# Kernel tuning notes

Hardware: AMD Instinct MI355X
Metric: run time of the kernel (lower is better)

The kernel has to match this reference:

```python
import jax, jax.numpy as jnp
import numpy as np

EMBED = 1024
SEQ = 2048
HEAD = 64
BATCH = 4


def setup_inputs() -> dict:
    key = jax.random.key(0)
    k1, k2, k3, k4 = jax.random.split(key, 4)
    # small weight scale to keep pre-softmax logits (scaled by sqrt(c)=32) stable
    x = jax.random.normal(k1, (BATCH, SEQ, EMBED), dtype=jnp.float32)
    Wk = jax.random.normal(k2, (HEAD, EMBED), dtype=jnp.float32) * 0.02
    Wq = jax.random.normal(k3, (HEAD, EMBED), dtype=jnp.float32) * 0.02
    Wv = jax.random.normal(k4, (HEAD, EMBED), dtype=jnp.float32) * 0.02
    return {"x": x, "Wk": Wk, "Wq": Wq, "Wv": Wv}


def reference(x, Wk, Wq, Wv):
    b, t, c = x.shape
    # nn.Linear(embed, head, bias=False): y = x @ W.T
    K = jnp.einsum('btc,hc->bth', x, Wk)
    Q = jnp.einsum('btc,hc->bth', x, Wq)
    V = jnp.einsum('btc,hc->bth', x, Wv)
    # NOTE: original multiplies by c**0.5 (not 1/sqrt) — faithful reproduction
    scores = jnp.einsum('bqh,bkh->bqk', Q, K) * (c ** 0.5)
    causal = jnp.tril(jnp.ones((t, t), dtype=bool))  # [t,t]
    scores = jnp.where(causal, scores, -jnp.inf)
    W = jax.nn.softmax(scores, axis=-1)
    # dropout = 0.0 (eval / deterministic)
    return jnp.einsum('bqk,bkh->bqh', W, V)
```

## Files before the change

### kernel.cpp

```cpp
#include <hip/hip_runtime.h>
#include <math.h>

#define EMBED 1024
#define SEQ   2048
#define HEAD  64
#define NROW  8192


typedef float f32x4  __attribute__((ext_vector_type(4)));
typedef short bf16x8 __attribute__((ext_vector_type(8)));

__device__ __forceinline__ ushort f2bf(float v) {
    union { float f; unsigned u; } t; t.f = v;
    unsigned r = t.u + 0x7FFFu + ((t.u >> 16) & 1u);
    return (ushort)(r >> 16);
}
__device__ __forceinline__ float bf2f(ushort h) {
    union { float f; unsigned u; } t; t.u = ((unsigned)h) << 16;
    return t.f;
}
__device__ __forceinline__ uint4 pack8(const ushort* o) {
    uint4 u;
    u.x = (unsigned)o[0] | ((unsigned)o[1] << 16);
    u.y = (unsigned)o[2] | ((unsigned)o[3] << 16);
    u.z = (unsigned)o[4] | ((unsigned)o[5] << 16);
    u.w = (unsigned)o[6] | ((unsigned)o[7] << 16);
    return u;
}

__global__ __launch_bounds__(256)
void prep_w(const float* __restrict__ Wq, const float* __restrict__ Wk,
            const float* __restrict__ Wv, ushort* __restrict__ Wt)
{
    const int id = blockIdx.x * 256 + threadIdx.x;
    const int g  = id / 2560;
    const int r1 = id - g * 2560;
    const int s  = r1 >> 6, l = r1 & 63;
    int f, hl, ks;
    if (s < 32) { f = s >> 2; hl = (s >> 1) & 1; ks = s & 1; }
    else        { int t = s - 32; f = 8 + (t >> 1); hl = 0; ks = t & 1; }
    const float* W = (f < 4) ? Wq : (f < 8) ? Wk : Wv;
    const int col = (f & 3) * 16 + (l & 15);
    const int k   = g * 64 + ks * 32 + (l >> 4) * 8;
    float4 v0 = *(const float4*)&W[(size_t)col * EMBED + k];
    float4 v1 = *(const float4*)&W[(size_t)col * EMBED + k + 4];
    const float vv[8] = {v0.x, v0.y, v0.z, v0.w, v1.x, v1.y, v1.z, v1.w};
    ushort o[8];
#pragma unroll
    for (int i = 0; i < 8; ++i) {
        const ushort h = f2bf(vv[i]);
        o[i] = hl ? f2bf(vv[i] - bf2f(h)) : h;
    }
    *(uint4*)&Wt[((size_t)g * 40 + s) * 512 + l * 8] = pack8(o);
}

__global__ __launch_bounds__(256)
void qkv_fused(const float* __restrict__ x, const ushort* __restrict__ Wt,
               ushort* __restrict__ Qh, ushort* __restrict__ Ql,
               ushort* __restrict__ Kh, ushort* __restrict__ Kl,
               ushort* __restrict__ Vr)
{
    __shared__ ushort SA[2][4 * 512];
    __shared__ float  T[3 * 16 * 68];

    const int tid  = threadIdx.x;
    const int w    = tid >> 6;
    const int lane = tid & 63;
    const int row0 = blockIdx.x * 16;

    const int  srow = tid >> 3, so8 = tid & 7;
    const int  sks  = so8 >> 2, soc = so8 & 3;
    const bool sact = (tid < 128);

    f32x4 acc[3];
#pragma unroll
    for (int fi = 0; fi < 3; ++fi) acc[fi] = (f32x4){0.f, 0.f, 0.f, 0.f};

    float4 xa, xb;
    if (sact) {
        const float* xp = &x[(size_t)(row0 + srow) * EMBED + so8 * 8];
        xa = *(const float4*)xp; xb = *(const float4*)(xp + 4);
        const float vv[8] = {xa.x, xa.y, xa.z, xa.w, xb.x, xb.y, xb.z, xb.w};
        ushort hs[8], ls[8];
#pragma unroll
        for (int i = 0; i < 8; ++i) { hs[i] = f2bf(vv[i]); ls[i] = f2bf(vv[i] - bf2f(hs[i])); }
        const int base = soc * 128 + srow * 8;
        *(uint4*)&SA[0][sks * 512 + base]       = pack8(hs);
        *(uint4*)&SA[0][(2 + sks) * 512 + base] = pack8(ls);
    }
    __syncthreads();

    for (int c = 0; c < 16; ++c) {
        const int cur = c & 1;
        if (c + 1 < 16 && sact) {
            const float* xp = &x[(size_t)(row0 + srow) * EMBED + (c + 1) * 64 + so8 * 8];
            xa = *(const float4*)xp; xb = *(const float4*)(xp + 4);
        }
        const ushort* Wg = &Wt[((size_t)c * 40) * 512 + lane * 8];
        bf16x8 qhf[2], qlf[2], khf[2], klf[2], vhf[2];
#pragma unroll
        for (int ks = 0; ks < 2; ++ks) {
            qhf[ks] = *(const bf16x8*)&Wg[(size_t)(w * 4 + ks) * 512];
            qlf[ks] = *(const bf16x8*)&Wg[(size_t)(w * 4 + 2 + ks) * 512];
            khf[ks] = *(const bf16x8*)&Wg[(size_t)((w + 4) * 4 + ks) * 512];
            klf[ks] = *(const bf16x8*)&Wg[(size_t)((w + 4) * 4 + 2 + ks) * 512];
            vhf[ks] = *(const bf16x8*)&Wg[(size_t)(32 + w * 2 + ks) * 512];
        }
#pragma unroll
        for (int ks = 0; ks < 2; ++ks) {
            bf16x8 ah = *(const bf16x8*)&SA[cur][ks * 512 + lane * 8];
            bf16x8 al = *(const bf16x8*)&SA[cur][(2 + ks) * 512 + lane * 8];
            acc[0] = __builtin_amdgcn_mfma_f32_16x16x32_bf16(ah, qhf[ks], acc[0], 0, 0, 0);
            acc[0] = __builtin_amdgcn_mfma_f32_16x16x32_bf16(ah, qlf[ks], acc[0], 0, 0, 0);
            acc[0] = __builtin_amdgcn_mfma_f32_16x16x32_bf16(al, qhf[ks], acc[0], 0, 0, 0);
            acc[1] = __builtin_amdgcn_mfma_f32_16x16x32_bf16(ah, khf[ks], acc[1], 0, 0, 0);
            acc[1] = __builtin_amdgcn_mfma_f32_16x16x32_bf16(ah, klf[ks], acc[1], 0, 0, 0);
            acc[1] = __builtin_amdgcn_mfma_f32_16x16x32_bf16(al, khf[ks], acc[1], 0, 0, 0);
            acc[2] = __builtin_amdgcn_mfma_f32_16x16x32_bf16(ah, vhf[ks], acc[2], 0, 0, 0);
        }
        if (c + 1 < 16 && sact) {
            const float vv[8] = {xa.x, xa.y, xa.z, xa.w, xb.x, xb.y, xb.z, xb.w};
            ushort hs[8], ls[8];
#pragma unroll
            for (int i = 0; i < 8; ++i) { hs[i] = f2bf(vv[i]); ls[i] = f2bf(vv[i] - bf2f(hs[i])); }
            const int base = soc * 128 + srow * 8;
            *(uint4*)&SA[cur ^ 1][sks * 512 + base]       = pack8(hs);
            *(uint4*)&SA[cur ^ 1][(2 + sks) * 512 + base] = pack8(ls);
        }
        __syncthreads();
    }

#pragma unroll
    for (int fi = 0; fi < 3; ++fi)
#pragma unroll
        for (int r = 0; r < 4; ++r)
            T[(fi * 16 + 4 * (lane >> 4) + r) * 68 + w * 16 + (lane & 15)] = acc[fi][r];
    __syncthreads();

    const int orow = tid >> 4, oc4 = tid & 15;
    const size_t obase = (size_t)(row0 + orow) * HEAD + oc4 * 4;
    {
        float4 v = *(const float4*)&T[(orow) * 68 + oc4 * 4];
        const float vv[4] = {32.f * v.x, 32.f * v.y, 32.f * v.z, 32.f * v.w};
        ushort h[4], l[4];
#pragma unroll
        for (int i = 0; i < 4; ++i) { h[i] = f2bf(vv[i]); l[i] = f2bf(vv[i] - bf2f(h[i])); }
        *(ushort4*)&Qh[obase] = make_ushort4(h[0], h[1], h[2], h[3]);
        *(ushort4*)&Ql[obase] = make_ushort4(l[0], l[1], l[2], l[3]);
    }
    {
        float4 v = *(const float4*)&T[(16 + orow) * 68 + oc4 * 4];
        const float vv[4] = {v.x, v.y, v.z, v.w};
        ushort h[4], l[4];
#pragma unroll
        for (int i = 0; i < 4; ++i) { h[i] = f2bf(vv[i]); l[i] = f2bf(vv[i] - bf2f(h[i])); }
        *(ushort4*)&Kh[obase] = make_ushort4(h[0], h[1], h[2], h[3]);
        *(ushort4*)&Kl[obase] = make_ushort4(l[0], l[1], l[2], l[3]);
    }
    {
        float4 v = *(const float4*)&T[(32 + orow) * 68 + oc4 * 4];
        *(ushort4*)&Vr[obase] =
            make_ushort4(f2bf(v.x), f2bf(v.y), f2bf(v.z), f2bf(v.w));
    }
}

__global__ __launch_bounds__(256)
void v_transpose(const ushort* __restrict__ Vr, ushort* __restrict__ Vt)
{
    __shared__ ushort T2[64][264];
    const int s  = blockIdx.x;
    const int b  = s >> 3;
    const int k0 = (s & 7) * 256;
    const int tid = threadIdx.x;
#pragma unroll
    for (int i = 0; i < 8; ++i) {
        const int u = tid + 256 * i;
        const int row = u >> 3, c8 = u & 7;
        uint4 v = *(const uint4*)&Vr[((size_t)(b * SEQ + k0 + row)) * HEAD + c8 * 8];
        const ushort* e = (const ushort*)&v;
#pragma unroll
        for (int j = 0; j < 8; ++j) T2[c8 * 8 + j][row] = e[j];
    }
    __syncthreads();
#pragma unroll
    for (int i = 0; i < 8; ++i) {
        const int u = tid + 256 * i;
        const int d = u >> 5, c8 = u & 31;
        uint4 val = *(const uint4*)&T2[d][c8 * 8];
        *(uint4*)&Vt[((size_t)(b * 64 + d)) * SEQ + k0 + c8 * 8] = val;
    }
}

__global__ __launch_bounds__(128)
void attn_mfma(const ushort* __restrict__ Qh, const ushort* __restrict__ Ql,
               const ushort* __restrict__ Kh, const ushort* __restrict__ Kl,
               const ushort* __restrict__ Vt, char* __restrict__ PO)
{
    const int id = blockIdx.x;
    const int b  = id / 160;
    const int f  = id - 160 * b;
    int G, u;
    if (f < 16)      { G = 0; u = f; }
    else if (f < 48) { G = 1; u = f - 16; }
    else if (f < 96) { G = 2; u = f - 48; }
    else             { G = 3; u = f - 96; }
    const int qb  = 16 * G + u / (G + 1);
    const int kc  = u % (G + 1);
    const int q0  = qb * 32;
    const int ktd = qb >> 1;
    const int nt  = ktd + 1;
    const int t0  = kc * 8;
    const int t1  = (t0 + 8 < nt) ? t0 + 8 : nt;

    const int tid = threadIdx.x;
    const int w   = tid >> 6;
    const int lane = tid & 63;
    const int g = lane >> 4, c = lane & 15;
    const int swz = (c & 7) << 3;

    __shared__ ushort KH[64 * 64];
    __shared__ ushort KL[64 * 64];
    __shared__ ushort VT[64 * 64];
    __shared__ ushort PS[2][16 * 64];

    const int qrow = q0 + 16 * w + c;
    bf16x8 qh[2], ql[2];
#pragma unroll
    for (int ks = 0; ks < 2; ++ks) {
        const size_t qi = ((size_t)(b * SEQ + qrow)) * HEAD + 32 * ks + 8 * g;
        qh[ks] = *(const bf16x8*)&Qh[qi];
        ql[ks] = *(const bf16x8*)&Ql[qi];
    }

    f32x4 o[4];
#pragma unroll
    for (int db = 0; db < 4; ++db) o[db] = (f32x4){0.f, 0.f, 0.f, 0.f};
    float m = -1e30f, lsum = 0.f;

    for (int kt = t0; kt < t1; ++kt) {
        const int kb0 = kt * 64;
        __syncthreads();
#pragma unroll
        for (int i = 0; i < 4; ++i) {
            const int u2  = tid + 128 * i;
            const int row = u2 >> 3, c8 = u2 & 7;
            const int dst = row * 64 + ((c8 ^ (row & 7)) * 8);
            const size_t ksrc = ((size_t)(b * SEQ + kb0 + row)) * HEAD + c8 * 8;
            *(uint4*)&KH[dst] = *(const uint4*)&Kh[ksrc];
            *(uint4*)&KL[dst] = *(const uint4*)&Kl[ksrc];
            const size_t vsrc = ((size_t)(b * 64 + row)) * SEQ + kb0 + c8 * 8;
            *(uint4*)&VT[dst] = *(const uint4*)&Vt[vsrc];
        }
        __syncthreads();

        f32x4 s[4];
#pragma unroll
        for (int kb = 0; kb < 4; ++kb) s[kb] = (f32x4){0.f, 0.f, 0.f, 0.f};
#pragma unroll
        for (int ks = 0; ks < 2; ++ks) {
            const int co = (32 * ks + 8 * g) ^ swz;
#pragma unroll
            for (int kb = 0; kb < 4; ++kb) {
                const int row = 16 * kb + c;
                bf16x8 ah = *(const bf16x8*)&KH[row * 64 + co];
                bf16x8 al = *(const bf16x8*)&KL[row * 64 + co];
                s[kb] = __builtin_amdgcn_mfma_f32_16x16x32_bf16(ah, qh[ks], s[kb], 0, 0, 0);
                s[kb] = __builtin_amdgcn_mfma_f32_16x16x32_bf16(ah, ql[ks], s[kb], 0, 0, 0);
                s[kb] = __builtin_amdgcn_mfma_f32_16x16x32_bf16(al, qh[ks], s[kb], 0, 0, 0);
            }
        }

        if (kt == ktd) {
#pragma unroll
            for (int kb = 0; kb < 4; ++kb)
#pragma unroll
                for (int r = 0; r < 4; ++r)
                    if (kb0 + 16 * kb + 4 * g + r > qrow) s[kb][r] = -1e30f;
        }

        float tmax = -1e30f;
#pragma unroll
        for (int kb = 0; kb < 4; ++kb) {
            float a = fmaxf(fmaxf(s[kb][0], s[kb][1]), fmaxf(s[kb][2], s[kb][3]));
            tmax = fmaxf(tmax, a);
        }
        tmax = fmaxf(tmax, __shfl_xor(tmax, 16));
        tmax = fmaxf(tmax, __shfl_xor(tmax, 32));
        const float mnew = fmaxf(m, tmax);
        const float fac  = __expf(m - mnew);
        float p[4][4];
        float psum = 0.f;
#pragma unroll
        for (int kb = 0; kb < 4; ++kb)
#pragma unroll
            for (int r = 0; r < 4; ++r) {
                p[kb][r] = __expf(s[kb][r] - mnew);
                psum += p[kb][r];
            }
        psum += __shfl_xor(psum, 16);
        psum += __shfl_xor(psum, 32);
        lsum = lsum * fac + psum;
        m = mnew;

        float fb[4];
#pragma unroll
        for (int r = 0; r < 4; ++r) fb[r] = __shfl(fac, 4 * g + r);
#pragma unroll
        for (int db = 0; db < 4; ++db) {
            o[db][0] *= fb[0]; o[db][1] *= fb[1];
            o[db][2] *= fb[2]; o[db][3] *= fb[3];
        }

#pragma unroll
        for (int kb = 0; kb < 4; ++kb) {
            const int idx = c * 64 + (((16 * kb + 4 * g)) ^ swz);
            *(ushort4*)&PS[w][idx] = make_ushort4(
                f2bf(p[kb][0]), f2bf(p[kb][1]), f2bf(p[kb][2]), f2bf(p[kb][3]));
        }

#pragma unroll
        for (int k2 = 0; k2 < 2; ++k2) {
            const int co = (32 * k2 + 8 * g) ^ swz;
            bf16x8 pa = *(const bf16x8*)&PS[w][c * 64 + co];
#pragma unroll
            for (int db = 0; db < 4; ++db) {
                const int row = 16 * db + c;
                bf16x8 vb = *(const bf16x8*)&VT[row * 64 + co];
                o[db] = __builtin_amdgcn_mfma_f32_16x16x32_bf16(pa, vb, o[db], 0, 0, 0);
            }
        }
    }

    char* item = PO + (size_t)id * 4352;
    ushort* po = (ushort*)item;
    float*  ml = (float*)(item + 4096);
    __syncthreads();
    ushort* OT = KH;
#pragma unroll
    for (int db = 0; db < 4; ++db)
#pragma unroll
        for (int r = 0; r < 4; ++r) {
            const int qq = 16 * w + 4 * g + r;
            OT[qq * 64 + 16 * db + c] = f2bf(o[db][r]);
        }
    if (g == 0) {
        ml[16 * w + c]      = m;
        ml[32 + 16 * w + c] = lsum;
    }
    __syncthreads();
#pragma unroll
    for (int i = 0; i < 2; ++i) {
        const int u2 = tid + 128 * i;
        *(uint4*)&po[u2 * 8] = *(const uint4*)&OT[u2 * 8];
    }
}

__global__ __launch_bounds__(256)
void attn_combine(const char* __restrict__ PO, float* __restrict__ out)
{
    const int qbg = blockIdx.x;
    const int b   = qbg >> 6, qb = qbg & 63;
    const int G   = qb >> 4, np = G + 1;
    const int base = b * 160 + (G + 1) * (qb - 8 * G);
    const int tid = threadIdx.x;
    const int row = tid >> 3, c8 = tid & 7;

    float M = -1e30f;
    for (int p = 0; p < np; ++p) {
        const float* ml = (const float*)(PO + (size_t)(base + p) * 4352 + 4096);
        M = fmaxf(M, ml[row]);
    }
    float L = 0.f;
    float acc[8];
#pragma unroll
    for (int j = 0; j < 8; ++j) acc[j] = 0.f;
    for (int p = 0; p < np; ++p) {
        const char* item = PO + (size_t)(base + p) * 4352;
        const float* ml  = (const float*)(item + 4096);
        const float wgt  = __expf(ml[row] - M);
        L += wgt * ml[32 + row];
        const ushort* po = (const ushort*)item;
        ushort4 a0 = *(const ushort4*)&po[row * 64 + c8 * 8];
        ushort4 a1 = *(const ushort4*)&po[row * 64 + c8 * 8 + 4];
        acc[0] += wgt * bf2f(a0.x); acc[1] += wgt * bf2f(a0.y);
        acc[2] += wgt * bf2f(a0.z); acc[3] += wgt * bf2f(a0.w);
        acc[4] += wgt * bf2f(a1.x); acc[5] += wgt * bf2f(a1.y);
        acc[6] += wgt * bf2f(a1.z); acc[7] += wgt * bf2f(a1.w);
    }
    const float inv = 1.f / L;
    float* dst = &out[((size_t)(b * SEQ + qb * 32 + row)) * HEAD + c8 * 8];
    *(float4*)dst       = make_float4(acc[0] * inv, acc[1] * inv, acc[2] * inv, acc[3] * inv);
    *(float4*)(dst + 4) = make_float4(acc[4] * inv, acc[5] * inv, acc[6] * inv, acc[7] * inv);
}


extern "C" void kernel_launch(void* const* d_in, const int* in_sizes, int n_in,
                              void* d_out, int out_size, void* d_ws, size_t ws_size,
                              hipStream_t stream)
{
    const float* x  = (const float*)d_in[0];
    const float* Wk = (const float*)d_in[1];
    const float* Wq = (const float*)d_in[2];
    const float* Wv = (const float*)d_in[3];

    char* ws = (char*)d_ws;
    ushort* Wt = (ushort*)ws;
    ushort* Qh = (ushort*)(ws +  655360);
    ushort* Ql = (ushort*)(ws + 1703936);
    ushort* Kh = (ushort*)(ws + 2752512);
    ushort* Kl = (ushort*)(ws + 3801088);
    ushort* Vr = (ushort*)(ws + 4849664);
    ushort* Vt = (ushort*)(ws + 5898240);
    char*   PO = ws + 6946816;

    prep_w      <<<dim3(160), 256, 0, stream>>>(Wq, Wk, Wv, Wt);
    qkv_fused   <<<dim3(512), 256, 0, stream>>>(x, Wt, Qh, Ql, Kh, Kl, Vr);
    v_transpose <<<dim3(32),  256, 0, stream>>>(Vr, Vt);
    attn_mfma   <<<dim3(640), 128, 0, stream>>>(Qh, Ql, Kh, Kl, Vt, PO);
    attn_combine<<<dim3(256), 256, 0, stream>>>(PO, (float*)d_out);
}
```

Baseline: 60.22 us.

## Double-buffer weight and K/V tile loads and split attention into finer KV chunks

In the QKV projection kernel, the weight fragments for the next chunk are now prefetched into registers while the current chunk's MFMAs run. In the attention kernel, K/V tiles are double-buffered in shared memory with register prefetch, so global loads overlap compute. The KV split is halved from 8 to 4 tiles per work item, which raises the grid from 640 to 1152 blocks, and the combine indexing is updated to match. This costs more registers and LDS per block and writes more partial results to combine.

Result: slower. 78.86 us (+30.9%).

```diff
diff --git a/kernel.cpp b/kernel.cpp
--- a/kernel.cpp
+++ b/kernel.cpp
@@ -76,49 +76,65 @@
 #pragma unroll
     for (int fi = 0; fi < 3; ++fi) acc[fi] = (f32x4){0.f, 0.f, 0.f, 0.f};
 
-    float4 xa, xb;
-    if (sact) {
+    bf16x8 wA[10], wB[10];
+
+    {
         const float* xp = &x[(size_t)(row0 + srow) * EMBED + so8 * 8];
-        xa = *(const float4*)xp; xb = *(const float4*)(xp + 4);
-        const float vv[8] = {xa.x, xa.y, xa.z, xa.w, xb.x, xb.y, xb.z, xb.w};
-        ushort hs[8], ls[8];
-#pragma unroll
-        for (int i = 0; i < 8; ++i) { hs[i] = f2bf(vv[i]); ls[i] = f2bf(vv[i] - bf2f(hs[i])); }
-        const int base = soc * 128 + srow * 8;
-        *(uint4*)&SA[0][sks * 512 + base]       = pack8(hs);
-        *(uint4*)&SA[0][(2 + sks) * 512 + base] = pack8(ls);
+        float4 xa, xb;
+        if (sact) { xa = *(const float4*)xp; xb = *(const float4*)(xp + 4); }
+        const ushort* Wg = &Wt[0 + lane * 8];
+#pragma unroll
+        for (int ks = 0; ks < 2; ++ks) {
+            wA[ks * 5 + 0] = *(const bf16x8*)&Wg[(size_t)(w * 4 + ks) * 512];
+            wA[ks * 5 + 1] = *(const bf16x8*)&Wg[(size_t)(w * 4 + 2 + ks) * 512];
+            wA[ks * 5 + 2] = *(const bf16x8*)&Wg[(size_t)((w + 4) * 4 + ks) * 512];
+            wA[ks * 5 + 3] = *(const bf16x8*)&Wg[(size_t)((w + 4) * 4 + 2 + ks) * 512];
+            wA[ks * 5 + 4] = *(const bf16x8*)&Wg[(size_t)(32 + w * 2 + ks) * 512];
+        }
+        if (sact) {
+            const float vv[8] = {xa.x, xa.y, xa.z, xa.w, xb.x, xb.y, xb.z, xb.w};
+            ushort hs[8], ls[8];
+#pragma unroll
+            for (int i = 0; i < 8; ++i) { hs[i] = f2bf(vv[i]); ls[i] = f2bf(vv[i] - bf2f(hs[i])); }
+            const int base = soc * 128 + srow * 8;
+            *(uint4*)&SA[0][sks * 512 + base]       = pack8(hs);
+            *(uint4*)&SA[0][(2 + sks) * 512 + base] = pack8(ls);
+        }
     }
     __syncthreads();
 
-    for (int c = 0; c < 16; ++c) {
+    auto chunk = [&](int c, bf16x8* wc, bf16x8* wn) {
         const int cur = c & 1;
-        if (c + 1 < 16 && sact) {
+        const bool pre = (c + 1 < 16);
+        float4 xa, xb;
+        if (pre && sact) {
             const float* xp = &x[(size_t)(row0 + srow) * EMBED + (c + 1) * 64 + so8 * 8];
             xa = *(const float4*)xp; xb = *(const float4*)(xp + 4);
         }
-        const ushort* Wg = &Wt[((size_t)c * 40) * 512 + lane * 8];
-        bf16x8 qhf[2], qlf[2], khf[2], klf[2], vhf[2];
-#pragma unroll
-        for (int ks = 0; ks < 2; ++ks) {
-            qhf[ks] = *(const bf16x8*)&Wg[(size_t)(w * 4 + ks) * 512];
-            qlf[ks] = *(const bf16x8*)&Wg[(size_t)(w * 4 + 2 + ks) * 512];
-            khf[ks] = *(const bf16x8*)&Wg[(size_t)((w + 4) * 4 + ks) * 512];
-            klf[ks] = *(const bf16x8*)&Wg[(size_t)((w + 4) * 4 + 2 + ks) * 512];
-            vhf[ks] = *(const bf16x8*)&Wg[(size_t)(32 + w * 2 + ks) * 512];
+        if (pre) {
+            const ushort* Wg = &Wt[((size_t)(c + 1) * 40) * 512 + lane * 8];
+#pragma unroll
+            for (int ks = 0; ks < 2; ++ks) {
+                wn[ks * 5 + 0] = *(const bf16x8*)&Wg[(size_t)(w * 4 + ks) * 512];
+                wn[ks * 5 + 1] = *(const bf16x8*)&Wg[(size_t)(w * 4 + 2 + ks) * 512];
+                wn[ks * 5 + 2] = *(const bf16x8*)&Wg[(size_t)((w + 4) * 4 + ks) * 512];
+                wn[ks * 5 + 3] = *(const bf16x8*)&Wg[(size_t)((w + 4) * 4 + 2 + ks) * 512];
+                wn[ks * 5 + 4] = *(const bf16x8*)&Wg[(size_t)(32 + w * 2 + ks) * 512];
+            }
         }
 #pragma unroll
         for (int ks = 0; ks < 2; ++ks) {
             bf16x8 ah = *(const bf16x8*)&SA[cur][ks * 512 + lane * 8];
             bf16x8 al = *(const bf16x8*)&SA[cur][(2 + ks) * 512 + lane * 8];
-            acc[0] = __builtin_amdgcn_mfma_f32_16x16x32_bf16(ah, qhf[ks], acc[0], 0, 0, 0);
-            acc[0] = __builtin_amdgcn_mfma_f32_16x16x32_bf16(ah, qlf[ks], acc[0], 0, 0, 0);
-            acc[0] = __builtin_amdgcn_mfma_f32_16x16x32_bf16(al, qhf[ks], acc[0], 0, 0, 0);
-            acc[1] = __builtin_amdgcn_mfma_f32_16x16x32_bf16(ah, khf[ks], acc[1], 0, 0, 0);
-            acc[1] = __builtin_amdgcn_mfma_f32_16x16x32_bf16(ah, klf[ks], acc[1], 0, 0, 0);
-            acc[1] = __builtin_amdgcn_mfma_f32_16x16x32_bf16(al, khf[ks], acc[1], 0, 0, 0);
-            acc[2] = __builtin_amdgcn_mfma_f32_16x16x32_bf16(ah, vhf[ks], acc[2], 0, 0, 0);
-        }
-        if (c + 1 < 16 && sact) {
+            acc[0] = __builtin_amdgcn_mfma_f32_16x16x32_bf16(ah, wc[ks * 5 + 0], acc[0], 0, 0, 0);
+            acc[0] = __builtin_amdgcn_mfma_f32_16x16x32_bf16(ah, wc[ks * 5 + 1], acc[0], 0, 0, 0);
+            acc[0] = __builtin_amdgcn_mfma_f32_16x16x32_bf16(al, wc[ks * 5 + 0], acc[0], 0, 0, 0);
+            acc[1] = __builtin_amdgcn_mfma_f32_16x16x32_bf16(ah, wc[ks * 5 + 2], acc[1], 0, 0, 0);
+            acc[1] = __builtin_amdgcn_mfma_f32_16x16x32_bf16(ah, wc[ks * 5 + 3], acc[1], 0, 0, 0);
+            acc[1] = __builtin_amdgcn_mfma_f32_16x16x32_bf16(al, wc[ks * 5 + 2], acc[1], 0, 0, 0);
+            acc[2] = __builtin_amdgcn_mfma_f32_16x16x32_bf16(ah, wc[ks * 5 + 4], acc[2], 0, 0, 0);
+        }
+        if (pre && sact) {
             const float vv[8] = {xa.x, xa.y, xa.z, xa.w, xb.x, xb.y, xb.z, xb.w};
             ushort hs[8], ls[8];
 #pragma unroll
@@ -128,6 +144,11 @@
             *(uint4*)&SA[cur ^ 1][(2 + sks) * 512 + base] = pack8(ls);
         }
         __syncthreads();
+    };
+
+    for (int cc = 0; cc < 16; cc += 2) {
+        chunk(cc,     wA, wB);
+        chunk(cc + 1, wB, wA);
     }
 
 #pragma unroll
@@ -197,20 +218,21 @@
                const ushort* __restrict__ Vt, char* __restrict__ PO)
 {
     const int id = blockIdx.x;
-    const int b  = id / 160;
-    const int f  = id - 160 * b;
-    int G, u;
-    if (f < 16)      { G = 0; u = f; }
-    else if (f < 48) { G = 1; u = f - 16; }
-    else if (f < 96) { G = 2; u = f - 48; }
-    else             { G = 3; u = f - 96; }
-    const int qb  = 16 * G + u / (G + 1);
-    const int kc  = u % (G + 1);
+    const int b  = id / 288;
+    int f = id - 288 * b;
+    int g2 = 0;
+    {
+        int base = 0;
+        while (f >= base + 8 * (g2 + 1)) { base += 8 * (g2 + 1); ++g2; }
+        f -= base;
+    }
+    const int qb  = 8 * g2 + f / (g2 + 1);
+    const int kc  = f - (g2 + 1) * (f / (g2 + 1));
     const int q0  = qb * 32;
     const int ktd = qb >> 1;
     const int nt  = ktd + 1;
-    const int t0  = kc * 8;
-    const int t1  = (t0 + 8 < nt) ? t0 + 8 : nt;
+    const int t0  = kc * 4;
+    const int t1  = (t0 + 4 < nt) ? t0 + 4 : nt;
 
     const int tid = threadIdx.x;
     const int w   = tid >> 6;
@@ -218,10 +240,13 @@
     const int g = lane >> 4, c = lane & 15;
     const int swz = (c & 7) << 3;
 
-    __shared__ ushort KH[64 * 64];
-    __shared__ ushort KL[64 * 64];
-    __shared__ ushort VT[64 * 64];
+    __shared__ ushort KH[2][64 * 64];
+    __shared__ ushort KL[2][64 * 64];
+    __shared__ ushort VT[2][64 * 64];
     __shared__ ushort PS[2][16 * 64];
+
+    const int srow = tid >> 3, sc8 = tid & 7;
+    const int sdst = srow * 64 + ((sc8 ^ (srow & 7)) * 8);
 
     const int qrow = q0 + 16 * w + c;
     bf16x8 qh[2], ql[2];
@@ -237,21 +262,40 @@
     for (int db = 0; db < 4; ++db) o[db] = (f32x4){0.f, 0.f, 0.f, 0.f};
     float m = -1e30f, lsum = 0.f;
 
+    uint4 kreg[4], lreg[4], vreg[4];
+#pragma unroll
+    for (int i = 0; i < 4; ++i) {
+        const int row = srow + 16 * i;
+        const size_t ksrc = ((size_t)(b * SEQ + t0 * 64 + row)) * HEAD + sc8 * 8;
+        kreg[i] = *(const uint4*)&Kh[ksrc];
+        lreg[i] = *(const uint4*)&Kl[ksrc];
+        const size_t vsrc = ((size_t)(b * 64 + row)) * SEQ + t0 * 64 + sc8 * 8;
+        vreg[i] = *(const uint4*)&Vt[vsrc];
+    }
+#pragma unroll
+    for (int i = 0; i < 4; ++i) {
+        const int dst = sdst + 16 * i * 64;
+        *(uint4*)&KH[0][dst] = kreg[i];
+        *(uint4*)&KL[0][dst] = lreg[i];
+        *(uint4*)&VT[0][dst] = vreg[i];
+    }
+    __syncthreads();
+
     for (int kt = t0; kt < t1; ++kt) {
+        const int cur = (kt - t0) & 1;
         const int kb0 = kt * 64;
-        __syncthreads();
-#pragma unroll
-        for (int i = 0; i < 4; ++i) {
-            const int u2  = tid + 128 * i;
-            const int row = u2 >> 3, c8 = u2 & 7;
-            const int dst = row * 64 + ((c8 ^ (row & 7)) * 8);
-            const size_t ksrc = ((size_t)(b * SEQ + kb0 + row)) * HEAD + c8 * 8;
-            *(uint4*)&KH[dst] = *(const uint4*)&Kh[ksrc];
-            *(uint4*)&KL[dst] = *(const uint4*)&Kl[ksrc];
-            const size_t vsrc = ((size_t)(b * 64 + row)) * SEQ + kb0 + c8 * 8;
-            *(uint4*)&VT[dst] = *(const uint4*)&Vt[vsrc];
-        }
-        __syncthreads();
+        const bool pre = (kt + 1 < t1);
+        if (pre) {
+#pragma unroll
+            for (int i = 0; i < 4; ++i) {
+                const int row = srow + 16 * i;
+                const size_t ksrc = ((size_t)(b * SEQ + kb0 + 64 + row)) * HEAD + sc8 * 8;
+                kreg[i] = *(const uint4*)&Kh[ksrc];
+                lreg[i] = *(const uint4*)&Kl[ksrc];
+                const size_t vsrc = ((size_t)(b * 64 + row)) * SEQ + kb0 + 64 + sc8 * 8;
+                vreg[i] = *(const uint4*)&Vt[vsrc];
+            }
+        }
 
         f32x4 s[4];
 #pragma unroll
@@ -262,8 +306,8 @@
 #pragma unroll
             for (int kb = 0; kb < 4; ++kb) {
                 const int row = 16 * kb + c;
-                bf16x8 ah = *(const bf16x8*)&KH[row * 64 + co];
-                bf16x8 al = *(const bf16x8*)&KL[row * 64 + co];
+                bf16x8 ah = *(const bf16x8*)&KH[cur][row * 64 + co];
+                bf16x8 al = *(const bf16x8*)&KL[cur][row * 64 + co];
                 s[kb] = __builtin_amdgcn_mfma_f32_16x16x32_bf16(ah, qh[ks], s[kb], 0, 0, 0);
                 s[kb] = __builtin_amdgcn_mfma_f32_16x16x32_bf16(ah, ql[ks], s[kb], 0, 0, 0);
                 s[kb] = __builtin_amdgcn_mfma_f32_16x16x32_bf16(al, qh[ks], s[kb], 0, 0, 0);
@@ -325,17 +369,27 @@
 #pragma unroll
             for (int db = 0; db < 4; ++db) {
                 const int row = 16 * db + c;
-                bf16x8 vb = *(const bf16x8*)&VT[row * 64 + co];
+                bf16x8 vb = *(const bf16x8*)&VT[cur][row * 64 + co];
                 o[db] = __builtin_amdgcn_mfma_f32_16x16x32_bf16(pa, vb, o[db], 0, 0, 0);
             }
         }
+
+        if (pre) {
+#pragma unroll
+            for (int i = 0; i < 4; ++i) {
+                const int dst = sdst + 16 * i * 64;
+                *(uint4*)&KH[cur ^ 1][dst] = kreg[i];
+                *(uint4*)&KL[cur ^ 1][dst] = lreg[i];
+                *(uint4*)&VT[cur ^ 1][dst] = vreg[i];
+            }
+        }
+        __syncthreads();
     }
 
     char* item = PO + (size_t)id * 4352;
     ushort* po = (ushort*)item;
     float*  ml = (float*)(item + 4096);
-    __syncthreads();
-    ushort* OT = KH;
+    ushort* OT = KH[0];
 #pragma unroll
     for (int db = 0; db < 4; ++db)
 #pragma unroll
@@ -360,8 +414,8 @@
 {
     const int qbg = blockIdx.x;
     const int b   = qbg >> 6, qb = qbg & 63;
-    const int G   = qb >> 4, np = G + 1;
-    const int base = b * 160 + (G + 1) * (qb - 8 * G);
+    const int g   = qb >> 3, np = g + 1;
+    const int base = b * 288 + 4 * g * (g + 1) + (qb - 8 * g) * (g + 1);
     const int tid = threadIdx.x;
     const int row = tid >> 3, c8 = tid & 7;
 
@@ -413,9 +467,9 @@
     ushort* Vt = (ushort*)(ws + 5898240);
     char*   PO = ws + 6946816;
 
-    prep_w      <<<dim3(160), 256, 0, stream>>>(Wq, Wk, Wv, Wt);
-    qkv_fused   <<<dim3(512), 256, 0, stream>>>(x, Wt, Qh, Ql, Kh, Kl, Vr);
-    v_transpose <<<dim3(32),  256, 0, stream>>>(Vr, Vt);
-    attn_mfma   <<<dim3(640), 128, 0, stream>>>(Qh, Ql, Kh, Kl, Vt, PO);
-    attn_combine<<<dim3(256), 256, 0, stream>>>(PO, (float*)d_out);
-}
+    prep_w      <<<dim3(160),  256, 0, stream>>>(Wq, Wk, Wv, Wt);
+    qkv_fused   <<<dim3(512),  256, 0, stream>>>(x, Wt, Qh, Ql, Kh, Kl, Vr);
+    v_transpose <<<dim3(32),   256, 0, stream>>>(Vr, Vt);
+    attn_mfma   <<<dim3(1152), 128, 0, stream>>>(Qh, Ql, Kh, Kl, Vt, PO);
+    attn_combine<<<dim3(256),  256, 0, stream>>>(PO, (float*)d_out);
+}
```
